# Kernel optimization log

Measured on AMD Instinct MI355X. Metric: run time of the kernel, lower is better.

Reference implementation:

```python
import math
import jax, jax.numpy as jnp
import numpy as np

N, S, D = 1024, 256, 256
C, R, CLASSES = 256, 64, 1000


def setup_inputs() -> dict:
    key = jax.random.key(0)
    ks = jax.random.split(key, 10)
    inv_sqrt_d = 1.0 / math.sqrt(D)
    return {
        "q": jax.random.normal(ks[0], (N, D), dtype=jnp.float32),
        "K": jax.random.normal(ks[1], (N, S, D), dtype=jnp.float32),
        "V": jax.random.normal(ks[2], (N, S, D), dtype=jnp.float32),
        "codebook": jax.random.normal(ks[3], (C, D), dtype=jnp.float32) * inv_sqrt_d,
        "residual_codebook": jax.random.normal(ks[4], (R, D), dtype=jnp.float32) * inv_sqrt_d,
        "Wq": jax.random.normal(ks[5], (D, D), dtype=jnp.float32) * inv_sqrt_d,
        "residual_logit": jnp.zeros((), dtype=jnp.float32),
        "Wc": jax.random.normal(ks[6], (CLASSES, D), dtype=jnp.float32) * inv_sqrt_d,
        "bc": jnp.zeros((CLASSES,), dtype=jnp.float32),
        "Wr": jax.random.normal(ks[7], (D, D), dtype=jnp.float32) * inv_sqrt_d,
        "br": jnp.zeros((D,), dtype=jnp.float32),
    }


def reference(q, K, V, codebook, residual_codebook, Wq, residual_logit, Wc, bc, Wr, br):
    scale = math.sqrt(q.shape[-1])
    q_proj = q @ Wq.T  # [N,D]

    # --- base codebook pass ---
    code_weights = jax.nn.softmax(jnp.einsum('nd,cd->nc', q_proj, codebook) / scale, axis=-1)
    slot_code_weights = jax.nn.softmax(jnp.einsum('nsd,cd->nsc', K, codebook) / scale, axis=-1)
    slot_code_summaries = jnp.einsum('nsc,nsd->ncd', slot_code_weights, V)
    base_summary = jnp.einsum('nc,ncd->nd', code_weights, slot_code_summaries)
    base_weights = jnp.einsum('nc,nsc->ns', code_weights, slot_code_weights)

    # --- residual quantization pass ---
    query_residual = q_proj - code_weights @ codebook
    slot_residual = K - jnp.einsum('nsc,cd->nsd', slot_code_weights, codebook)
    residual_code_weights = jax.nn.softmax(
        jnp.einsum('nd,rd->nr', query_residual, residual_codebook) / scale, axis=-1)
    residual_slot_code_weights = jax.nn.softmax(
        jnp.einsum('nsd,rd->nsr', slot_residual, residual_codebook) / scale, axis=-1)
    residual_slot_summaries = jnp.einsum('nsr,nsd->nrd', residual_slot_code_weights, V)
    residual_summary = jnp.einsum('nr,nrd->nd', residual_code_weights, residual_slot_summaries)
    residual_weights = jnp.einsum('nr,nsr->ns', residual_code_weights, residual_slot_code_weights)

    gate = jax.nn.sigmoid(residual_logit)
    summary = base_summary + gate * residual_summary
    effective_weights = (base_weights + gate * residual_weights) / (1.0 + gate)

    logits = summary @ Wc.T + bc
    recon = summary @ Wr.T + br
    return (logits, recon, effective_weights)
```

## Files before the change

kernel.cpp:

```cpp
#include <hip/hip_runtime.h>
#include <hip/hip_bf16.h>
#include <math.h>

#define N_   1024
#define S_   256
#define D_   256
#define C_   256
#define R_   64
#define CLS_ 1000
#define INV16 0.0625f

typedef unsigned short ushortT;
typedef unsigned int uint32;
typedef short bf8 __attribute__((ext_vector_type(8)));
typedef float f4 __attribute__((ext_vector_type(4)));

static __device__ __forceinline__ float bf2f(uint32 u){
  return __uint_as_float(u << 16);
}
static __device__ __forceinline__ ushortT f2bf(float f){
  uint32 x = __float_as_uint(f);
  uint32 r = x + 0x7FFFu + ((x >> 16) & 1u);
  return (ushortT)(r >> 16);
}
static __device__ __forceinline__ uint32 packbf(float a, float b){
  return ((uint32)f2bf(b) << 16) | (uint32)f2bf(a);
}
static __device__ __forceinline__ float wred_max(float v){
  for (int o = 32; o; o >>= 1) v = fmaxf(v, __shfl_xor(v, o));
  return v;
}
static __device__ __forceinline__ float wred_sum(float v){
  for (int o = 32; o; o >>= 1) v += __shfl_xor(v, o);
  return v;
}
static __device__ __forceinline__ int swz(int row, int colbyte){
  return row*512 + ((colbyte & ~15) ^ ((row & 7) << 4)) + (colbyte & 15);
}
static __device__ __forceinline__ int pkidx(int row, int col, int nfrag){
  int ks = col >> 5, hi = (col >> 3) & 3, e = col & 7;
  int frag = row >> 4, l15p = row & 15;
  return ((ks*nfrag + frag)*64 + hi*16 + l15p)*8 + e;
}

__global__ __launch_bounds__(256) void k0(const float* __restrict__ cb,
    const float* __restrict__ rcb, const float* __restrict__ Wc,
    const float* __restrict__ Wr, ushortT* __restrict__ a1pk,
    ushortT* __restrict__ Wcr_bf, float* __restrict__ MT_f32,
    ushortT* __restrict__ mtpk)
{
  __shared__ float rl[D_];
  int bid = blockIdx.x, t = threadIdx.x;
  int gtid = bid*256 + t;
  int stride = gridDim.x*256;
  for (int e = gtid; e < (C_ + R_)*D_; e += stride){
    int row = e >> 8, col = e & 255;
    float v = (row < C_) ? cb[e] : rcb[e - C_*D_];
    a1pk[pkidx(row, col, 20)] = f2bf(v);
  }
  for (int e = gtid; e < CLS_*D_; e += stride) Wcr_bf[e] = f2bf(Wc[e]);
  for (int e = gtid; e < D_*D_; e += stride)  Wcr_bf[CLS_*D_ + e] = f2bf(Wr[e]);
  for (int e = gtid; e < 24*D_; e += stride)  Wcr_bf[1256*D_ + e] = 0;

  if (bid < R_){
    rl[t] = rcb[bid*D_ + t];
    __syncthreads();
    float acc = 0.f;
    const float* crow = cb + t*D_;
    #pragma unroll 8
    for (int k = 0; k < D_; k += 4){
      float4 w = *(const float4*)(crow + k);
      acc += w.x*rl[k] + w.y*rl[k+1] + w.z*rl[k+2] + w.w*rl[k+3];
    }
    MT_f32[bid*C_ + t] = acc;
    mtpk[pkidx(bid, t, 4)] = f2bf(acc);
  }
}

#define G4 4
__global__ __launch_bounds__(256) void k1(const float* __restrict__ q,
    const float* __restrict__ cb, const float* __restrict__ rcb,
    const float* __restrict__ Wq, const float* __restrict__ MT_f32,
    float* __restrict__ cw_ws, float* __restrict__ rcw_ws)
{
  __shared__ float qv[G4][D_], qp[G4][D_], cwl[G4][C_];
  __shared__ float redA[G4][4], redB2[G4][4];
  int n0 = blockIdx.x*G4, t = threadIdx.x;
  #pragma unroll
  for (int g = 0; g < G4; g++) qv[g][t] = q[(n0+g)*D_ + t];
  __syncthreads();
  {
    float acc[G4] = {0.f,0.f,0.f,0.f};
    const float* wrow = Wq + t*D_;
    #pragma unroll 4
    for (int k = 0; k < D_; k += 4){
      float4 w = *(const float4*)(wrow + k);
      #pragma unroll
      for (int g = 0; g < G4; g++)
        acc[g] += qv[g][k]*w.x + qv[g][k+1]*w.y + qv[g][k+2]*w.z + qv[g][k+3]*w.w;
    }
    #pragma unroll
    for (int g = 0; g < G4; g++) qp[g][t] = acc[g];
  }
  __syncthreads();
  float L[G4] = {0.f,0.f,0.f,0.f};
  {
    const float* crow = cb + t*D_;
    #pragma unroll 4
    for (int k = 0; k < D_; k += 4){
      float4 w = *(const float4*)(crow + k);
      #pragma unroll
      for (int g = 0; g < G4; g++)
        L[g] += qp[g][k]*w.x + qp[g][k+1]*w.y + qp[g][k+2]*w.z + qp[g][k+3]*w.w;
    }
  }
  float m[G4], e[G4], s[G4];
  #pragma unroll
  for (int g = 0; g < G4; g++){ L[g] *= INV16; m[g] = wred_max(L[g]); }
  if ((t & 63) == 0)
    #pragma unroll
    for (int g = 0; g < G4; g++) redA[g][t >> 6] = m[g];
  __syncthreads();
  #pragma unroll
  for (int g = 0; g < G4; g++){
    m[g] = fmaxf(fmaxf(redA[g][0], redA[g][1]), fmaxf(redA[g][2], redA[g][3]));
    e[g] = __expf(L[g] - m[g]);
    s[g] = wred_sum(e[g]);
  }
  if ((t & 63) == 0)
    #pragma unroll
    for (int g = 0; g < G4; g++) redB2[g][t >> 6] = s[g];
  __syncthreads();
  #pragma unroll
  for (int g = 0; g < G4; g++){
    float ss = redB2[g][0] + redB2[g][1] + redB2[g][2] + redB2[g][3];
    float w = e[g] / ss;
    cwl[g][t] = w;
    cw_ws[(n0+g)*C_ + t] = w;
  }
  __syncthreads();
  if (t < R_){
    float qd[G4] = {0.f,0.f,0.f,0.f}, md[G4] = {0.f,0.f,0.f,0.f};
    const float* rrow = rcb + t*D_;
    const float* mrow = MT_f32 + t*C_;
    #pragma unroll 4
    for (int k = 0; k < D_; k += 4){
      float4 wv = *(const float4*)(rrow + k);
      float4 mv = *(const float4*)(mrow + k);
      #pragma unroll
      for (int g = 0; g < G4; g++){
        qd[g] += qp[g][k]*wv.x + qp[g][k+1]*wv.y + qp[g][k+2]*wv.z + qp[g][k+3]*wv.w;
        md[g] += cwl[g][k]*mv.x + cwl[g][k+1]*mv.y + cwl[g][k+2]*mv.z + cwl[g][k+3]*mv.w;
      }
    }
    #pragma unroll
    for (int g = 0; g < G4; g++){
      float Lr = (qd[g] - md[g]) * INV16;
      float mr = wred_max(Lr);
      float er = __expf(Lr - mr);
      float sr = wred_sum(er);
      rcw_ws[(n0+g)*R_ + t] = er / sr;
    }
  }
}

__global__ __launch_bounds__(256) void k2a(const float* __restrict__ Kt,
    const ushortT* __restrict__ a1pk, const ushortT* __restrict__ mtpk,
    const float* __restrict__ cw_ws, const float* __restrict__ rcw_ws,
    const float* __restrict__ rlogit, float* __restrict__ comb_ws,
    float* __restrict__ out_ew)
{
  __shared__ __align__(16) ushortT KW[64*256];
  __shared__ float redS[4][64], redW[4][64];

  int bx  = blockIdx.x;
  int n   = bx >> 2;
  int s0  = (bx & 3) * 64;
  int tid = threadIdx.x;
  int lane = tid & 63, w = tid >> 6;
  int l15 = lane & 15, l4 = lane >> 4;
  float gate  = 1.f / (1.f + __expf(-rlogit[0]));
  float inv1g = 1.f / (1.f + gate);

  const float* Kn = Kt + (size_t)n*S_*D_ + (size_t)s0*D_;

  #pragma unroll
  for (int j = 0; j < 8; j++){
    int ch = tid + j*256;
    int row = ch >> 5, blk = ch & 31;
    const float* src = Kn + row*D_ + blk*8;
    float4 a = *(const float4*)src;
    float4 b = *(const float4*)(src + 4);
    uint4 wv = {packbf(a.x,a.y), packbf(a.z,a.w), packbf(b.x,b.y), packbf(b.z,b.w)};
    *(uint4*)((char*)KW + swz(row, blk*16)) = wv;
  }
  __syncthreads();

  const ushortT* a1b = a1pk + (size_t)lane*8;
  bf8 bnxC[4], bnxR[4];
  #pragma unroll
  for (int f = 0; f < 4; f++){
    bnxC[f] = *(const bf8*)(a1b + (size_t)((w + 4*f)*64)*8);
    bnxR[f] = *(const bf8*)(a1b + (size_t)((16 + f)*64)*8);
  }
  f4 accC[4][4]; f4 accR[4];
  #pragma unroll
  for (int f = 0; f < 4; f++){
    accR[f] = (f4)0.f;
    #pragma unroll
    for (int sj = 0; sj < 4; sj++) accC[f][sj] = (f4)0.f;
  }
  #pragma unroll
  for (int ks = 0; ks < 8; ks++){
    bf8 kf0 = *(const bf8*)((const char*)KW + swz(     l15, ks*64 + l4*16));
    bf8 kf1 = *(const bf8*)((const char*)KW + swz(16 + l15, ks*64 + l4*16));
    bf8 kf2 = *(const bf8*)((const char*)KW + swz(32 + l15, ks*64 + l4*16));
    bf8 kf3 = *(const bf8*)((const char*)KW + swz(48 + l15, ks*64 + l4*16));
    bf8 kfw = *(const bf8*)((const char*)KW + swz(w*16 + l15, ks*64 + l4*16));
    #pragma unroll
    for (int f = 0; f < 4; f++){
      bf8 aC = bnxC[f], aR = bnxR[f];
      if (ks < 7){
        bnxC[f] = *(const bf8*)(a1b + (size_t)(((ks+1)*20 + w + 4*f)*64)*8);
        bnxR[f] = *(const bf8*)(a1b + (size_t)(((ks+1)*20 + 16 + f)*64)*8);
      }
      accC[f][0] = __builtin_amdgcn_mfma_f32_16x16x32_bf16(aC, kf0, accC[f][0], 0, 0, 0);
      accC[f][1] = __builtin_amdgcn_mfma_f32_16x16x32_bf16(aC, kf1, accC[f][1], 0, 0, 0);
      accC[f][2] = __builtin_amdgcn_mfma_f32_16x16x32_bf16(aC, kf2, accC[f][2], 0, 0, 0);
      accC[f][3] = __builtin_amdgcn_mfma_f32_16x16x32_bf16(aC, kf3, accC[f][3], 0, 0, 0);
      accR[f]    = __builtin_amdgcn_mfma_f32_16x16x32_bf16(aR, kfw, accR[f],    0, 0, 0);
    }
  }

  float4 cwv[4];
  #pragma unroll
  for (int f = 0; f < 4; f++)
    cwv[f] = *(const float4*)(cw_ws + n*C_ + (w + 4*f)*16 + l4*4);
  float se[4] = {0,0,0,0}, sb[4] = {0,0,0,0};
  #pragma unroll
  for (int f = 0; f < 4; f++)
    #pragma unroll
    for (int sj = 0; sj < 4; sj++){
      float e0 = __expf(accC[f][sj][0] * INV16);
      float e1 = __expf(accC[f][sj][1] * INV16);
      float e2 = __expf(accC[f][sj][2] * INV16);
      float e3 = __expf(accC[f][sj][3] * INV16);
      accC[f][sj][0] = e0; accC[f][sj][1] = e1;
      accC[f][sj][2] = e2; accC[f][sj][3] = e3;
      se[sj] += (e0 + e1) + (e2 + e3);
      sb[sj] += e0*cwv[f].x + e1*cwv[f].y + e2*cwv[f].z + e3*cwv[f].w;
    }
  #pragma unroll
  for (int sj = 0; sj < 4; sj++){
    se[sj] += __shfl_xor(se[sj], 16); se[sj] += __shfl_xor(se[sj], 32);
    sb[sj] += __shfl_xor(sb[sj], 16); sb[sj] += __shfl_xor(sb[sj], 32);
  }
  if (l4 == 0){
    #pragma unroll
    for (int sj = 0; sj < 4; sj++){
      redS[w][sj*16 + l15] = se[sj];
      redW[w][sj*16 + l15] = sb[sj];
    }
  }
  __syncthreads();

  float bw_q, rcp_q;
  {
    int sq = w*16 + l15;
    float sS = redS[0][sq] + redS[1][sq] + redS[2][sq] + redS[3][sq];
    float sW = redW[0][sq] + redW[1][sq] + redW[2][sq] + redW[3][sq];
    bw_q  = sW / sS;
    rcp_q = 1.f / sS;
  }
  #pragma unroll
  for (int f = 0; f < 4; f++){
    int cbyte = ((w + 4*f)*16 + l4*4) * 2;
    #pragma unroll
    for (int sj = 0; sj < 4; sj++){
      int s_ = sj*16 + l15;
      *(uint32*)((char*)KW + swz(s_, cbyte))     = packbf(accC[f][sj][0], accC[f][sj][1]);
      *(uint32*)((char*)KW + swz(s_, cbyte + 4)) = packbf(accC[f][sj][2], accC[f][sj][3]);
    }
  }
  __syncthreads();

  const ushortT* mtb = mtpk + (size_t)lane*8;
  bf8 mnx[4];
  #pragma unroll
  for (int fr = 0; fr < 4; fr++)
    mnx[fr] = *(const bf8*)(mtb + (size_t)(fr*64)*8);
  f4 wm[4];
  #pragma unroll
  for (int fr = 0; fr < 4; fr++) wm[fr] = (f4)0.f;
  #pragma unroll
  for (int ks = 0; ks < 8; ks++){
    bf8 wb = *(const bf8*)((const char*)KW + swz(w*16 + l15, ks*64 + l4*16));
    #pragma unroll
    for (int fr = 0; fr < 4; fr++){
      bf8 a = mnx[fr];
      if (ks < 7) mnx[fr] = *(const bf8*)(mtb + (size_t)(((ks+1)*4 + fr)*64)*8);
      wm[fr] = __builtin_amdgcn_mfma_f32_16x16x32_bf16(a, wb, wm[fr], 0, 0, 0);
    }
  }

  float4 rcwv[4];
  #pragma unroll
  for (int fr = 0; fr < 4; fr++)
    rcwv[fr] = *(const float4*)(rcw_ws + n*R_ + fr*16 + l4*4);
  float se3 = 0.f, sc3 = 0.f;
  #pragma unroll
  for (int fr = 0; fr < 4; fr++){
    float e0 = __expf((accR[fr][0] - wm[fr][0]*rcp_q) * INV16);
    float e1 = __expf((accR[fr][1] - wm[fr][1]*rcp_q) * INV16);
    float e2 = __expf((accR[fr][2] - wm[fr][2]*rcp_q) * INV16);
    float e3 = __expf((accR[fr][3] - wm[fr][3]*rcp_q) * INV16);
    se3 += (e0 + e1) + (e2 + e3);
    sc3 += e0*rcwv[fr].x + e1*rcwv[fr].y + e2*rcwv[fr].z + e3*rcwv[fr].w;
  }
  se3 += __shfl_xor(se3, 16); se3 += __shfl_xor(se3, 32);
  sc3 += __shfl_xor(sc3, 16); sc3 += __shfl_xor(sc3, 32);
  float comb = bw_q + gate * (sc3 / se3);
  if (l4 == 0){
    int sabs = n*S_ + s0 + w*16 + l15;
    out_ew[sabs]  = comb * inv1g;
    comb_ws[sabs] = comb;
  }
}

__global__ __launch_bounds__(256) void k2b(const float* __restrict__ Vt,
    const float* __restrict__ comb_ws, float* __restrict__ sum_ws)
{
  __shared__ float cl[S_];
  __shared__ float4 part[4][64];
  int n = blockIdx.x, tid = threadIdx.x;
  int lane = tid & 63, w = tid >> 6;
  cl[tid] = comb_ws[n*S_ + tid];
  __syncthreads();
  const float* Vn = Vt + (size_t)n*S_*D_ + (size_t)(w*64)*D_ + lane*4;
  float4 a0 = {0,0,0,0}, a1 = {0,0,0,0};
  #pragma unroll 8
  for (int j = 0; j < 64; j += 2){
    float4 v0 = *(const float4*)(Vn + (size_t)j*D_);
    float4 v1 = *(const float4*)(Vn + (size_t)(j+1)*D_);
    float c0 = cl[w*64 + j], c1 = cl[w*64 + j + 1];
    a0.x = fmaf(c0, v0.x, a0.x); a0.y = fmaf(c0, v0.y, a0.y);
    a0.z = fmaf(c0, v0.z, a0.z); a0.w = fmaf(c0, v0.w, a0.w);
    a1.x = fmaf(c1, v1.x, a1.x); a1.y = fmaf(c1, v1.y, a1.y);
    a1.z = fmaf(c1, v1.z, a1.z); a1.w = fmaf(c1, v1.w, a1.w);
  }
  float4 acc = {a0.x+a1.x, a0.y+a1.y, a0.z+a1.z, a0.w+a1.w};
  part[w][lane] = acc;
  __syncthreads();
  if (tid < 64){
    float4 p0 = part[0][tid], p1 = part[1][tid], p2 = part[2][tid], p3 = part[3][tid];
    float4 r = {p0.x+p1.x+p2.x+p3.x, p0.y+p1.y+p2.y+p3.y,
                p0.z+p1.z+p2.z+p3.z, p0.w+p1.w+p2.w+p3.w};
    *(float4*)(sum_ws + (size_t)n*D_ + tid*4) = r;
  }
}

__global__ __launch_bounds__(256) void k3(const float* __restrict__ sum_ws,
    const ushortT* __restrict__ Wcr_bf, const float* __restrict__ bc,
    const float* __restrict__ br, float* __restrict__ out)
{
  __shared__ __align__(16) ushortT Stile[64*256];
  int bx = blockIdx.x;
  int ot = bx >> 4;
  int nt = bx & 15;
  int tid = threadIdx.x;
  int lane = tid & 63, wid = tid >> 6;
  int l15 = lane & 15, l4 = lane >> 4;

  const float* Sp = sum_ws + (size_t)nt*64*D_;
  #pragma unroll
  for (int j = 0; j < 8; j++){
    int ch = tid + j*256;
    int row = ch >> 5, blk = ch & 31;
    const float* src = Sp + row*D_ + blk*8;
    float4 a = *(const float4*)src;
    float4 b = *(const float4*)(src + 4);
    uint4 wv = {packbf(a.x,a.y), packbf(a.z,a.w), packbf(b.x,b.y), packbf(b.z,b.w)};
    *(uint4*)((char*)Stile + swz(row, blk*16)) = wv;
  }
  __syncthreads();

  int o0 = ot*64 + wid*16;
  const ushortT* Ap = Wcr_bf + (size_t)(o0 + l15)*D_ + l4*8;
  f4 acc[4];
  #pragma unroll
  for (int j = 0; j < 4; j++) acc[j] = (f4)0.f;
  #pragma unroll
  for (int k = 0; k < 8; k++){
    bf8 a = *(const bf8*)(Ap + k*32);
    #pragma unroll
    for (int nj = 0; nj < 4; nj++){
      bf8 b = *(const bf8*)((const char*)Stile + swz(nj*16 + l15, k*64 + l4*16));
      acc[nj] = __builtin_amdgcn_mfma_f32_16x16x32_bf16(a, b, acc[nj], 0, 0, 0);
    }
  }
  int obase = o0 + l4*4;
  if (obase < 1256){
    float4 bias;
    if (obase < CLS_) bias = *(const float4*)(bc + obase);
    else              bias = *(const float4*)(br + (obase - CLS_));
    #pragma unroll
    for (int nj = 0; nj < 4; nj++){
      int nn = nt*64 + nj*16 + l15;
      float4 v = {acc[nj][0]+bias.x, acc[nj][1]+bias.y, acc[nj][2]+bias.z, acc[nj][3]+bias.w};
      if (obase < CLS_) *(float4*)(out + (size_t)nn*CLS_ + obase) = v;
      else              *(float4*)(out + (size_t)N_*CLS_ + (size_t)nn*D_ + (obase - CLS_)) = v;
    }
  }
}

extern "C" void kernel_launch(void* const* d_in, const int* in_sizes, int n_in,
                              void* d_out, int out_size, void* d_ws, size_t ws_size,
                              hipStream_t stream)
{
  const float* q    = (const float*)d_in[0];
  const float* Kt   = (const float*)d_in[1];
  const float* Vt   = (const float*)d_in[2];
  const float* cb   = (const float*)d_in[3];
  const float* rcb  = (const float*)d_in[4];
  const float* Wq   = (const float*)d_in[5];
  const float* rlg  = (const float*)d_in[6];
  const float* Wc   = (const float*)d_in[7];
  const float* bc   = (const float*)d_in[8];
  const float* Wr   = (const float*)d_in[9];
  const float* br   = (const float*)d_in[10];
  float* out = (float*)d_out;
  float* ws  = (float*)d_ws;

  float* cw_ws   = ws;
  float* rcw_ws  = ws + 262144;
  float* sum_ws  = ws + 327680;
  float* comb_ws = ws + 589824;
  float* MT_f32  = ws + 851968;
  ushortT* a1pk   = (ushortT*)(ws + 868352);
  ushortT* mtpk   = a1pk + (C_ + R_)*D_;
  ushortT* Wcr_bf = mtpk + R_*C_;

  float* out_logits = out;
  float* out_ew     = out + (size_t)N_*CLS_ + (size_t)N_*D_;

  k0 <<<128,   256, 0, stream>>>(cb, rcb, Wc, Wr, a1pk, Wcr_bf, MT_f32, mtpk);
  k1 <<<N_/G4, 256, 0, stream>>>(q, cb, rcb, Wq, MT_f32, cw_ws, rcw_ws);
  k2a<<<N_*4,  256, 0, stream>>>(Kt, a1pk, mtpk, cw_ws, rcw_ws, rlg, comb_ws, out_ew);
  k2b<<<N_,    256, 0, stream>>>(Vt, comb_ws, sum_ws);
  k3 <<<320,   256, 0, stream>>>(sum_ws, Wcr_bf, bc, br, out_logits);
}
```

Before: 234.4 us.

## Fuse V-weighted summary into k2a via atomics and repartition residual MFMA work

Removes the separate k2b kernel and the comb_ws round trip: each k2a block now multiplies its 64 slots' combined weights against V and atomically adds partial summaries into sum_ws, which k0 zero-initialises. The residual-code MFMAs are also repartitioned so each wave owns 16 residual codes across all 64 slots instead of 16 slots across all codes. A cross-wave reduction through shared memory with one extra barrier replaces the per-wave softmax normalisation. This saves a launch and a pass over comb_ws, at the cost of 4-way float atomics per output element and nondeterministic summation order.

After: 288.3 us. 23.0% more time.

```diff
diff --git a/kernel.cpp b/kernel.cpp
--- a/kernel.cpp
+++ b/kernel.cpp
@@ -47,7 +47,7 @@
     const float* __restrict__ rcb, const float* __restrict__ Wc,
     const float* __restrict__ Wr, ushortT* __restrict__ a1pk,
     ushortT* __restrict__ Wcr_bf, float* __restrict__ MT_f32,
-    ushortT* __restrict__ mtpk)
+    ushortT* __restrict__ mtpk, float* __restrict__ sum_ws)
 {
   __shared__ float rl[D_];
   int bid = blockIdx.x, t = threadIdx.x;
@@ -61,6 +61,7 @@
   for (int e = gtid; e < CLS_*D_; e += stride) Wcr_bf[e] = f2bf(Wc[e]);
   for (int e = gtid; e < D_*D_; e += stride)  Wcr_bf[CLS_*D_ + e] = f2bf(Wr[e]);
   for (int e = gtid; e < 24*D_; e += stride)  Wcr_bf[1256*D_ + e] = 0;
+  for (int e = gtid; e < N_*D_; e += stride)  sum_ws[e] = 0.f;
 
   if (bid < R_){
     rl[t] = rcb[bid*D_ + t];
@@ -165,10 +166,10 @@
 }
 
 __global__ __launch_bounds__(256) void k2a(const float* __restrict__ Kt,
-    const ushortT* __restrict__ a1pk, const ushortT* __restrict__ mtpk,
-    const float* __restrict__ cw_ws, const float* __restrict__ rcw_ws,
-    const float* __restrict__ rlogit, float* __restrict__ comb_ws,
-    float* __restrict__ out_ew)
+    const float* __restrict__ Vt, const ushortT* __restrict__ a1pk,
+    const ushortT* __restrict__ mtpk, const float* __restrict__ cw_ws,
+    const float* __restrict__ rcw_ws, const float* __restrict__ rlogit,
+    float* __restrict__ sum_ws, float* __restrict__ out_ew)
 {
   __shared__ __align__(16) ushortT KW[64*256];
   __shared__ float redS[4][64], redW[4][64];
@@ -184,6 +185,12 @@
 
   const float* Kn = Kt + (size_t)n*S_*D_ + (size_t)s0*D_;
 
+  const ushortT* aRb = a1pk + (size_t)((16 + w)*64 + lane)*8;
+  bf8 bR[8];
+  #pragma unroll
+  for (int ks = 0; ks < 8; ks++)
+    bR[ks] = *(const bf8*)(aRb + (size_t)(ks*20*64)*8);
+
   #pragma unroll
   for (int j = 0; j < 8; j++){
     int ch = tid + j*256;
@@ -197,12 +204,10 @@
   __syncthreads();
 
   const ushortT* a1b = a1pk + (size_t)lane*8;
-  bf8 bnxC[4], bnxR[4];
-  #pragma unroll
-  for (int f = 0; f < 4; f++){
+  bf8 bnxC[4];
+  #pragma unroll
+  for (int f = 0; f < 4; f++)
     bnxC[f] = *(const bf8*)(a1b + (size_t)((w + 4*f)*64)*8);
-    bnxR[f] = *(const bf8*)(a1b + (size_t)((16 + f)*64)*8);
-  }
   f4 accC[4][4]; f4 accR[4];
   #pragma unroll
   for (int f = 0; f < 4; f++){
@@ -216,21 +221,27 @@
     bf8 kf1 = *(const bf8*)((const char*)KW + swz(16 + l15, ks*64 + l4*16));
     bf8 kf2 = *(const bf8*)((const char*)KW + swz(32 + l15, ks*64 + l4*16));
     bf8 kf3 = *(const bf8*)((const char*)KW + swz(48 + l15, ks*64 + l4*16));
-    bf8 kfw = *(const bf8*)((const char*)KW + swz(w*16 + l15, ks*64 + l4*16));
     #pragma unroll
     for (int f = 0; f < 4; f++){
-      bf8 aC = bnxC[f], aR = bnxR[f];
-      if (ks < 7){
+      bf8 aC = bnxC[f];
+      if (ks < 7)
         bnxC[f] = *(const bf8*)(a1b + (size_t)(((ks+1)*20 + w + 4*f)*64)*8);
-        bnxR[f] = *(const bf8*)(a1b + (size_t)(((ks+1)*20 + 16 + f)*64)*8);
-      }
       accC[f][0] = __builtin_amdgcn_mfma_f32_16x16x32_bf16(aC, kf0, accC[f][0], 0, 0, 0);
       accC[f][1] = __builtin_amdgcn_mfma_f32_16x16x32_bf16(aC, kf1, accC[f][1], 0, 0, 0);
       accC[f][2] = __builtin_amdgcn_mfma_f32_16x16x32_bf16(aC, kf2, accC[f][2], 0, 0, 0);
       accC[f][3] = __builtin_amdgcn_mfma_f32_16x16x32_bf16(aC, kf3, accC[f][3], 0, 0, 0);
-      accR[f]    = __builtin_amdgcn_mfma_f32_16x16x32_bf16(aR, kfw, accR[f],    0, 0, 0);
-    }
-  }
+    }
+    accR[0] = __builtin_amdgcn_mfma_f32_16x16x32_bf16(bR[ks], kf0, accR[0], 0, 0, 0);
+    accR[1] = __builtin_amdgcn_mfma_f32_16x16x32_bf16(bR[ks], kf1, accR[1], 0, 0, 0);
+    accR[2] = __builtin_amdgcn_mfma_f32_16x16x32_bf16(bR[ks], kf2, accR[2], 0, 0, 0);
+    accR[3] = __builtin_amdgcn_mfma_f32_16x16x32_bf16(bR[ks], kf3, accR[3], 0, 0, 0);
+  }
+
+  const ushortT* mtb = mtpk + (size_t)(w*64 + lane)*8;
+  bf8 mnx[8];
+  #pragma unroll
+  for (int ks = 0; ks < 8; ks++)
+    mnx[ks] = *(const bf8*)(mtb + (size_t)(ks*4*64)*8);
 
   float4 cwv[4];
   #pragma unroll
@@ -264,13 +275,18 @@
   }
   __syncthreads();
 
-  float bw_q, rcp_q;
+  float rcp[4];
+  #pragma unroll
+  for (int sj = 0; sj < 4; sj++){
+    int s_ = sj*16 + l15;
+    rcp[sj] = 1.f / (redS[0][s_] + redS[1][s_] + redS[2][s_] + redS[3][s_]);
+  }
+  float bw_q;
   {
     int sq = w*16 + l15;
     float sS = redS[0][sq] + redS[1][sq] + redS[2][sq] + redS[3][sq];
     float sW = redW[0][sq] + redW[1][sq] + redW[2][sq] + redW[3][sq];
-    bw_q  = sW / sS;
-    rcp_q = 1.f / sS;
+    bw_q = sW / sS;
   }
   #pragma unroll
   for (int f = 0; f < 4; f++){
@@ -284,78 +300,68 @@
   }
   __syncthreads();
 
-  const ushortT* mtb = mtpk + (size_t)lane*8;
-  bf8 mnx[4];
-  #pragma unroll
-  for (int fr = 0; fr < 4; fr++)
-    mnx[fr] = *(const bf8*)(mtb + (size_t)(fr*64)*8);
   f4 wm[4];
   #pragma unroll
-  for (int fr = 0; fr < 4; fr++) wm[fr] = (f4)0.f;
+  for (int sj = 0; sj < 4; sj++) wm[sj] = (f4)0.f;
   #pragma unroll
   for (int ks = 0; ks < 8; ks++){
-    bf8 wb = *(const bf8*)((const char*)KW + swz(w*16 + l15, ks*64 + l4*16));
-    #pragma unroll
-    for (int fr = 0; fr < 4; fr++){
-      bf8 a = mnx[fr];
-      if (ks < 7) mnx[fr] = *(const bf8*)(mtb + (size_t)(((ks+1)*4 + fr)*64)*8);
-      wm[fr] = __builtin_amdgcn_mfma_f32_16x16x32_bf16(a, wb, wm[fr], 0, 0, 0);
-    }
-  }
-
-  float4 rcwv[4];
-  #pragma unroll
-  for (int fr = 0; fr < 4; fr++)
-    rcwv[fr] = *(const float4*)(rcw_ws + n*R_ + fr*16 + l4*4);
-  float se3 = 0.f, sc3 = 0.f;
-  #pragma unroll
-  for (int fr = 0; fr < 4; fr++){
-    float e0 = __expf((accR[fr][0] - wm[fr][0]*rcp_q) * INV16);
-    float e1 = __expf((accR[fr][1] - wm[fr][1]*rcp_q) * INV16);
-    float e2 = __expf((accR[fr][2] - wm[fr][2]*rcp_q) * INV16);
-    float e3 = __expf((accR[fr][3] - wm[fr][3]*rcp_q) * INV16);
-    se3 += (e0 + e1) + (e2 + e3);
-    sc3 += e0*rcwv[fr].x + e1*rcwv[fr].y + e2*rcwv[fr].z + e3*rcwv[fr].w;
-  }
-  se3 += __shfl_xor(se3, 16); se3 += __shfl_xor(se3, 32);
-  sc3 += __shfl_xor(sc3, 16); sc3 += __shfl_xor(sc3, 32);
-  float comb = bw_q + gate * (sc3 / se3);
+    bf8 wb0 = *(const bf8*)((const char*)KW + swz(     l15, ks*64 + l4*16));
+    bf8 wb1 = *(const bf8*)((const char*)KW + swz(16 + l15, ks*64 + l4*16));
+    bf8 wb2 = *(const bf8*)((const char*)KW + swz(32 + l15, ks*64 + l4*16));
+    bf8 wb3 = *(const bf8*)((const char*)KW + swz(48 + l15, ks*64 + l4*16));
+    wm[0] = __builtin_amdgcn_mfma_f32_16x16x32_bf16(mnx[ks], wb0, wm[0], 0, 0, 0);
+    wm[1] = __builtin_amdgcn_mfma_f32_16x16x32_bf16(mnx[ks], wb1, wm[1], 0, 0, 0);
+    wm[2] = __builtin_amdgcn_mfma_f32_16x16x32_bf16(mnx[ks], wb2, wm[2], 0, 0, 0);
+    wm[3] = __builtin_amdgcn_mfma_f32_16x16x32_bf16(mnx[ks], wb3, wm[3], 0, 0, 0);
+  }
+
+  float4 rcwv = *(const float4*)(rcw_ws + n*R_ + w*16 + l4*4);
+  float se3[4], sc3[4];
+  #pragma unroll
+  for (int sj = 0; sj < 4; sj++){
+    float e0 = __expf((accR[sj][0] - wm[sj][0]*rcp[sj]) * INV16);
+    float e1 = __expf((accR[sj][1] - wm[sj][1]*rcp[sj]) * INV16);
+    float e2 = __expf((accR[sj][2] - wm[sj][2]*rcp[sj]) * INV16);
+    float e3 = __expf((accR[sj][3] - wm[sj][3]*rcp[sj]) * INV16);
+    float s_e = (e0 + e1) + (e2 + e3);
+    float s_c = e0*rcwv.x + e1*rcwv.y + e2*rcwv.z + e3*rcwv.w;
+    s_e += __shfl_xor(s_e, 16); s_e += __shfl_xor(s_e, 32);
+    s_c += __shfl_xor(s_c, 16); s_c += __shfl_xor(s_c, 32);
+    se3[sj] = s_e; sc3[sj] = s_c;
+  }
   if (l4 == 0){
-    int sabs = n*S_ + s0 + w*16 + l15;
-    out_ew[sabs]  = comb * inv1g;
-    comb_ws[sabs] = comb;
-  }
-}
-
-__global__ __launch_bounds__(256) void k2b(const float* __restrict__ Vt,
-    const float* __restrict__ comb_ws, float* __restrict__ sum_ws)
-{
-  __shared__ float cl[S_];
-  __shared__ float4 part[4][64];
-  int n = blockIdx.x, tid = threadIdx.x;
-  int lane = tid & 63, w = tid >> 6;
-  cl[tid] = comb_ws[n*S_ + tid];
-  __syncthreads();
-  const float* Vn = Vt + (size_t)n*S_*D_ + (size_t)(w*64)*D_ + lane*4;
-  float4 a0 = {0,0,0,0}, a1 = {0,0,0,0};
-  #pragma unroll 8
-  for (int j = 0; j < 64; j += 2){
-    float4 v0 = *(const float4*)(Vn + (size_t)j*D_);
-    float4 v1 = *(const float4*)(Vn + (size_t)(j+1)*D_);
-    float c0 = cl[w*64 + j], c1 = cl[w*64 + j + 1];
-    a0.x = fmaf(c0, v0.x, a0.x); a0.y = fmaf(c0, v0.y, a0.y);
-    a0.z = fmaf(c0, v0.z, a0.z); a0.w = fmaf(c0, v0.w, a0.w);
-    a1.x = fmaf(c1, v1.x, a1.x); a1.y = fmaf(c1, v1.y, a1.y);
-    a1.z = fmaf(c1, v1.z, a1.z); a1.w = fmaf(c1, v1.w, a1.w);
-  }
-  float4 acc = {a0.x+a1.x, a0.y+a1.y, a0.z+a1.z, a0.w+a1.w};
-  part[w][lane] = acc;
-  __syncthreads();
-  if (tid < 64){
-    float4 p0 = part[0][tid], p1 = part[1][tid], p2 = part[2][tid], p3 = part[3][tid];
-    float4 r = {p0.x+p1.x+p2.x+p3.x, p0.y+p1.y+p2.y+p3.y,
-                p0.z+p1.z+p2.z+p3.z, p0.w+p1.w+p2.w+p3.w};
-    *(float4*)(sum_ws + (size_t)n*D_ + tid*4) = r;
+    #pragma unroll
+    for (int sj = 0; sj < 4; sj++){
+      redS[w][sj*16 + l15] = se3[sj];
+      redW[w][sj*16 + l15] = sc3[sj];
+    }
+  }
+  __syncthreads();
+
+  float comb;
+  {
+    int sq = w*16 + l15;
+    float sS = redS[0][sq] + redS[1][sq] + redS[2][sq] + redS[3][sq];
+    float sW = redW[0][sq] + redW[1][sq] + redW[2][sq] + redW[3][sq];
+    comb = bw_q + gate * (sW / sS);
+    if (l4 == 0) out_ew[n*S_ + s0 + sq] = comb * inv1g;
+  }
+
+  {
+    const float* vp = Vt + (size_t)n*S_*D_ + (size_t)(s0 + w*16)*D_ + lane*4;
+    float4 sacc = {0.f, 0.f, 0.f, 0.f};
+    #pragma unroll
+    for (int j = 0; j < 16; j++){
+      float cj = __shfl(comb, j);
+      float4 v = *(const float4*)(vp + (size_t)j*D_);
+      sacc.x = fmaf(cj, v.x, sacc.x); sacc.y = fmaf(cj, v.y, sacc.y);
+      sacc.z = fmaf(cj, v.z, sacc.z); sacc.w = fmaf(cj, v.w, sacc.w);
+    }
+    float* dst = sum_ws + (size_t)n*D_ + lane*4;
+    atomicAdd(dst + 0, sacc.x);
+    atomicAdd(dst + 1, sacc.y);
+    atomicAdd(dst + 2, sacc.z);
+    atomicAdd(dst + 3, sacc.w);
   }
 }
 
@@ -434,18 +440,16 @@
   float* cw_ws   = ws;
   float* rcw_ws  = ws + 262144;
   float* sum_ws  = ws + 327680;
-  float* comb_ws = ws + 589824;
-  float* MT_f32  = ws + 851968;
-  ushortT* a1pk   = (ushortT*)(ws + 868352);
+  float* MT_f32  = ws + 589824;
+  ushortT* a1pk   = (ushortT*)(ws + 606208);
   ushortT* mtpk   = a1pk + (C_ + R_)*D_;
   ushortT* Wcr_bf = mtpk + R_*C_;
 
   float* out_logits = out;
   float* out_ew     = out + (size_t)N_*CLS_ + (size_t)N_*D_;
 
-  k0 <<<128,   256, 0, stream>>>(cb, rcb, Wc, Wr, a1pk, Wcr_bf, MT_f32, mtpk);
+  k0 <<<128,   256, 0, stream>>>(cb, rcb, Wc, Wr, a1pk, Wcr_bf, MT_f32, mtpk, sum_ws);
   k1 <<<N_/G4, 256, 0, stream>>>(q, cb, rcb, Wq, MT_f32, cw_ws, rcw_ws);
-  k2a<<<N_*4,  256, 0, stream>>>(Kt, a1pk, mtpk, cw_ws, rcw_ws, rlg, comb_ws, out_ew);
-  k2b<<<N_,    256, 0, stream>>>(Vt, comb_ws, sum_ws);
+  k2a<<<N_*4,  256, 0, stream>>>(Kt, Vt, a1pk, mtpk, cw_ws, rcw_ws, rlg, sum_ws, out_ew);
   k3 <<<320,   256, 0, stream>>>(sum_ws, Wcr_bf, bc, br, out_logits);
 }
```

## Loop k2a over slot tiles with double-buffered LDS K prefetch

Applied to the files above, without the earlier changes.

k2a now launches one block per query row instead of four, looping over the four 64-slot tiles. The next tile of K is loaded from global memory into registers during the current tile's MFMA loop, then converted to bf16 and stored into a second LDS buffer. The per-row cw/rcw vectors are loaded once per block instead of once per tile. This hides global-load latency behind compute, but the doubled LDS footprint and a quarter of the blocks may reduce occupancy and latency hiding across blocks.

Result: slower. 493.4 us (+110.4%).

```diff
diff --git a/kernel.cpp b/kernel.cpp
--- a/kernel.cpp
+++ b/kernel.cpp
@@ -170,160 +170,207 @@
     const float* __restrict__ rlogit, float* __restrict__ comb_ws,
     float* __restrict__ out_ew)
 {
-  __shared__ __align__(16) ushortT KW[64*256];
+  __shared__ __align__(16) ushortT KW[2][64*256];
   __shared__ float redS[4][64], redW[4][64];
 
-  int bx  = blockIdx.x;
-  int n   = bx >> 2;
-  int s0  = (bx & 3) * 64;
+  int n   = blockIdx.x;
   int tid = threadIdx.x;
   int lane = tid & 63, w = tid >> 6;
   int l15 = lane & 15, l4 = lane >> 4;
   float gate  = 1.f / (1.f + __expf(-rlogit[0]));
   float inv1g = 1.f / (1.f + gate);
 
-  const float* Kn = Kt + (size_t)n*S_*D_ + (size_t)s0*D_;
+  const float* KnBase = Kt + (size_t)n*S_*D_;
+
+  float4 cwv[4];
+  #pragma unroll
+  for (int f = 0; f < 4; f++)
+    cwv[f] = *(const float4*)(cw_ws + n*C_ + (w + 4*f)*16 + l4*4);
+  float4 rcwv[4];
+  #pragma unroll
+  for (int fr = 0; fr < 4; fr++)
+    rcwv[fr] = *(const float4*)(rcw_ws + n*R_ + fr*16 + l4*4);
 
   #pragma unroll
   for (int j = 0; j < 8; j++){
     int ch = tid + j*256;
     int row = ch >> 5, blk = ch & 31;
-    const float* src = Kn + row*D_ + blk*8;
+    const float* src = KnBase + row*D_ + blk*8;
     float4 a = *(const float4*)src;
     float4 b = *(const float4*)(src + 4);
     uint4 wv = {packbf(a.x,a.y), packbf(a.z,a.w), packbf(b.x,b.y), packbf(b.z,b.w)};
-    *(uint4*)((char*)KW + swz(row, blk*16)) = wv;
-  }
-  __syncthreads();
-
-  const ushortT* a1b = a1pk + (size_t)lane*8;
-  bf8 bnxC[4], bnxR[4];
-  #pragma unroll
-  for (int f = 0; f < 4; f++){
-    bnxC[f] = *(const bf8*)(a1b + (size_t)((w + 4*f)*64)*8);
-    bnxR[f] = *(const bf8*)(a1b + (size_t)((16 + f)*64)*8);
-  }
-  f4 accC[4][4]; f4 accR[4];
-  #pragma unroll
-  for (int f = 0; f < 4; f++){
-    accR[f] = (f4)0.f;
-    #pragma unroll
-    for (int sj = 0; sj < 4; sj++) accC[f][sj] = (f4)0.f;
-  }
-  #pragma unroll
-  for (int ks = 0; ks < 8; ks++){
-    bf8 kf0 = *(const bf8*)((const char*)KW + swz(     l15, ks*64 + l4*16));
-    bf8 kf1 = *(const bf8*)((const char*)KW + swz(16 + l15, ks*64 + l4*16));
-    bf8 kf2 = *(const bf8*)((const char*)KW + swz(32 + l15, ks*64 + l4*16));
-    bf8 kf3 = *(const bf8*)((const char*)KW + swz(48 + l15, ks*64 + l4*16));
-    bf8 kfw = *(const bf8*)((const char*)KW + swz(w*16 + l15, ks*64 + l4*16));
+    *(uint4*)((char*)KW[0] + swz(row, blk*16)) = wv;
+  }
+  __syncthreads();
+
+  #pragma unroll 1
+  for (int t = 0; t < 4; t++){
+    int s0 = t*64;
+    const char* KWc = (const char*)KW[t & 1];
+    char*       KWn = (char*)KW[(t & 1) ^ 1];
+    const float* Knx = KnBase + (size_t)(s0 + 64)*D_;
+    bool stage = (t < 3);
+
+    const ushortT* a1b = a1pk + (size_t)lane*8;
+    bf8 bnxC[4], bnxR[4];
     #pragma unroll
     for (int f = 0; f < 4; f++){
-      bf8 aC = bnxC[f], aR = bnxR[f];
-      if (ks < 7){
-        bnxC[f] = *(const bf8*)(a1b + (size_t)(((ks+1)*20 + w + 4*f)*64)*8);
-        bnxR[f] = *(const bf8*)(a1b + (size_t)(((ks+1)*20 + 16 + f)*64)*8);
-      }
-      accC[f][0] = __builtin_amdgcn_mfma_f32_16x16x32_bf16(aC, kf0, accC[f][0], 0, 0, 0);
-      accC[f][1] = __builtin_amdgcn_mfma_f32_16x16x32_bf16(aC, kf1, accC[f][1], 0, 0, 0);
-      accC[f][2] = __builtin_amdgcn_mfma_f32_16x16x32_bf16(aC, kf2, accC[f][2], 0, 0, 0);
-      accC[f][3] = __builtin_amdgcn_mfma_f32_16x16x32_bf16(aC, kf3, accC[f][3], 0, 0, 0);
-      accR[f]    = __builtin_amdgcn_mfma_f32_16x16x32_bf16(aR, kfw, accR[f],    0, 0, 0);
-    }
-  }
-
-  float4 cwv[4];
-  #pragma unroll
-  for (int f = 0; f < 4; f++)
-    cwv[f] = *(const float4*)(cw_ws + n*C_ + (w + 4*f)*16 + l4*4);
-  float se[4] = {0,0,0,0}, sb[4] = {0,0,0,0};
-  #pragma unroll
-  for (int f = 0; f < 4; f++)
+      bnxC[f] = *(const bf8*)(a1b + (size_t)((w + 4*f)*64)*8);
+      bnxR[f] = *(const bf8*)(a1b + (size_t)((16 + f)*64)*8);
+    }
+    f4 accC[4][4]; f4 accR[4];
+    #pragma unroll
+    for (int f = 0; f < 4; f++){
+      accR[f] = (f4)0.f;
+      #pragma unroll
+      for (int sj = 0; sj < 4; sj++) accC[f][sj] = (f4)0.f;
+    }
+    float4 stg[2][2];
+    #pragma unroll
+    for (int ks = 0; ks < 8; ks++){
+      if (stage){
+        if (ks >= 2){
+          int j = ks - 2;
+          int ch = tid + j*256;
+          int row = ch >> 5, blk = ch & 31;
+          uint4 wv = {packbf(stg[j & 1][0].x, stg[j & 1][0].y),
+                      packbf(stg[j & 1][0].z, stg[j & 1][0].w),
+                      packbf(stg[j & 1][1].x, stg[j & 1][1].y),
+                      packbf(stg[j & 1][1].z, stg[j & 1][1].w)};
+          *(uint4*)(KWn + swz(row, blk*16)) = wv;
+        }
+        {
+          int ch = tid + ks*256;
+          int row = ch >> 5, blk = ch & 31;
+          const float* src = Knx + row*D_ + blk*8;
+          stg[ks & 1][0] = *(const float4*)src;
+          stg[ks & 1][1] = *(const float4*)(src + 4);
+        }
+      }
+      bf8 kf0 = *(const bf8*)(KWc + swz(     l15, ks*64 + l4*16));
+      bf8 kf1 = *(const bf8*)(KWc + swz(16 + l15, ks*64 + l4*16));
+      bf8 kf2 = *(const bf8*)(KWc + swz(32 + l15, ks*64 + l4*16));
+      bf8 kf3 = *(const bf8*)(KWc + swz(48 + l15, ks*64 + l4*16));
+      bf8 kfw = *(const bf8*)(KWc + swz(w*16 + l15, ks*64 + l4*16));
+      #pragma unroll
+      for (int f = 0; f < 4; f++){
+        bf8 aC = bnxC[f], aR = bnxR[f];
+        if (ks < 7){
+          bnxC[f] = *(const bf8*)(a1b + (size_t)(((ks+1)*20 + w + 4*f)*64)*8);
+          bnxR[f] = *(const bf8*)(a1b + (size_t)(((ks+1)*20 + 16 + f)*64)*8);
+        }
+        accC[f][0] = __builtin_amdgcn_mfma_f32_16x16x32_bf16(aC, kf0, accC[f][0], 0, 0, 0);
+        accC[f][1] = __builtin_amdgcn_mfma_f32_16x16x32_bf16(aC, kf1, accC[f][1], 0, 0, 0);
+        accC[f][2] = __builtin_amdgcn_mfma_f32_16x16x32_bf16(aC, kf2, accC[f][2], 0, 0, 0);
+        accC[f][3] = __builtin_amdgcn_mfma_f32_16x16x32_bf16(aC, kf3, accC[f][3], 0, 0, 0);
+        accR[f]    = __builtin_amdgcn_mfma_f32_16x16x32_bf16(aR, kfw, accR[f],    0, 0, 0);
+      }
+    }
+    if (stage){
+      #pragma unroll
+      for (int j = 6; j < 8; j++){
+        int ch = tid + j*256;
+        int row = ch >> 5, blk = ch & 31;
+        uint4 wv = {packbf(stg[j & 1][0].x, stg[j & 1][0].y),
+                    packbf(stg[j & 1][0].z, stg[j & 1][0].w),
+                    packbf(stg[j & 1][1].x, stg[j & 1][1].y),
+                    packbf(stg[j & 1][1].z, stg[j & 1][1].w)};
+        *(uint4*)(KWn + swz(row, blk*16)) = wv;
+      }
+    }
+
+    float se[4] = {0,0,0,0}, sb[4] = {0,0,0,0};
+    #pragma unroll
+    for (int f = 0; f < 4; f++)
+      #pragma unroll
+      for (int sj = 0; sj < 4; sj++){
+        float e0 = __expf(accC[f][sj][0] * INV16);
+        float e1 = __expf(accC[f][sj][1] * INV16);
+        float e2 = __expf(accC[f][sj][2] * INV16);
+        float e3 = __expf(accC[f][sj][3] * INV16);
+        accC[f][sj][0] = e0; accC[f][sj][1] = e1;
+        accC[f][sj][2] = e2; accC[f][sj][3] = e3;
+        se[sj] += (e0 + e1) + (e2 + e3);
+        sb[sj] += e0*cwv[f].x + e1*cwv[f].y + e2*cwv[f].z + e3*cwv[f].w;
+      }
     #pragma unroll
     for (int sj = 0; sj < 4; sj++){
-      float e0 = __expf(accC[f][sj][0] * INV16);
-      float e1 = __expf(accC[f][sj][1] * INV16);
-      float e2 = __expf(accC[f][sj][2] * INV16);
-      float e3 = __expf(accC[f][sj][3] * INV16);
-      accC[f][sj][0] = e0; accC[f][sj][1] = e1;
-      accC[f][sj][2] = e2; accC[f][sj][3] = e3;
-      se[sj] += (e0 + e1) + (e2 + e3);
-      sb[sj] += e0*cwv[f].x + e1*cwv[f].y + e2*cwv[f].z + e3*cwv[f].w;
-    }
-  #pragma unroll
-  for (int sj = 0; sj < 4; sj++){
-    se[sj] += __shfl_xor(se[sj], 16); se[sj] += __shfl_xor(se[sj], 32);
-    sb[sj] += __shfl_xor(sb[sj], 16); sb[sj] += __shfl_xor(sb[sj], 32);
-  }
-  if (l4 == 0){
-    #pragma unroll
-    for (int sj = 0; sj < 4; sj++){
-      redS[w][sj*16 + l15] = se[sj];
-      redW[w][sj*16 + l15] = sb[sj];
-    }
-  }
-  __syncthreads();
-
-  float bw_q, rcp_q;
-  {
-    int sq = w*16 + l15;
-    float sS = redS[0][sq] + redS[1][sq] + redS[2][sq] + redS[3][sq];
-    float sW = redW[0][sq] + redW[1][sq] + redW[2][sq] + redW[3][sq];
-    bw_q  = sW / sS;
-    rcp_q = 1.f / sS;
-  }
-  #pragma unroll
-  for (int f = 0; f < 4; f++){
-    int cbyte = ((w + 4*f)*16 + l4*4) * 2;
+      se[sj] += __shfl_xor(se[sj], 16); se[sj] += __shfl_xor(se[sj], 32);
+      sb[sj] += __shfl_xor(sb[sj], 16); sb[sj] += __shfl_xor(sb[sj], 32);
+    }
+    if (l4 == 0){
+      #pragma unroll
+      for (int sj = 0; sj < 4; sj++){
+        redS[w][sj*16 + l15] = se[sj];
+        redW[w][sj*16 + l15] = sb[sj];
+      }
+    }
+    __syncthreads();
+
+    float rcp[4];
     #pragma unroll
     for (int sj = 0; sj < 4; sj++){
       int s_ = sj*16 + l15;
-      *(uint32*)((char*)KW + swz(s_, cbyte))     = packbf(accC[f][sj][0], accC[f][sj][1]);
-      *(uint32*)((char*)KW + swz(s_, cbyte + 4)) = packbf(accC[f][sj][2], accC[f][sj][3]);
-    }
-  }
-  __syncthreads();
-
-  const ushortT* mtb = mtpk + (size_t)lane*8;
-  bf8 mnx[4];
-  #pragma unroll
-  for (int fr = 0; fr < 4; fr++)
-    mnx[fr] = *(const bf8*)(mtb + (size_t)(fr*64)*8);
-  f4 wm[4];
-  #pragma unroll
-  for (int fr = 0; fr < 4; fr++) wm[fr] = (f4)0.f;
-  #pragma unroll
-  for (int ks = 0; ks < 8; ks++){
-    bf8 wb = *(const bf8*)((const char*)KW + swz(w*16 + l15, ks*64 + l4*16));
+      rcp[sj] = 1.f / (redS[0][s_] + redS[1][s_] + redS[2][s_] + redS[3][s_]);
+    }
+    float bw_q, rcp_q;
+    {
+      int sq = w*16 + l15;
+      float sS = redS[0][sq] + redS[1][sq] + redS[2][sq] + redS[3][sq];
+      float sW = redW[0][sq] + redW[1][sq] + redW[2][sq] + redW[3][sq];
+      bw_q  = sW / sS;
+      rcp_q = 1.f / sS;
+    }
+    #pragma unroll
+    for (int f = 0; f < 4; f++){
+      int cbyte = ((w + 4*f)*16 + l4*4) * 2;
+      #pragma unroll
+      for (int sj = 0; sj < 4; sj++){
+        int s_ = sj*16 + l15;
+        *(uint32*)((char*)KWc + swz(s_, cbyte))     = packbf(accC[f][sj][0], accC[f][sj][1]);
+        *(uint32*)((char*)KWc + swz(s_, cbyte + 4)) = packbf(accC[f][sj][2], accC[f][sj][3]);
+      }
+    }
+    __syncthreads();
+
+    const ushortT* mtb = mtpk + (size_t)lane*8;
+    bf8 mnx[4];
+    #pragma unroll
+    for (int fr = 0; fr < 4; fr++)
+      mnx[fr] = *(const bf8*)(mtb + (size_t)(fr*64)*8);
+    f4 wm[4];
+    #pragma unroll
+    for (int fr = 0; fr < 4; fr++) wm[fr] = (f4)0.f;
+    #pragma unroll
+    for (int ks = 0; ks < 8; ks++){
+      bf8 wb = *(const bf8*)(KWc + swz(w*16 + l15, ks*64 + l4*16));
+      #pragma unroll
+      for (int fr = 0; fr < 4; fr++){
+        bf8 a = mnx[fr];
+        if (ks < 7) mnx[fr] = *(const bf8*)(mtb + (size_t)(((ks+1)*4 + fr)*64)*8);
+        wm[fr] = __builtin_amdgcn_mfma_f32_16x16x32_bf16(a, wb, wm[fr], 0, 0, 0);
+      }
+    }
+
+    float se3 = 0.f, sc3 = 0.f;
     #pragma unroll
     for (int fr = 0; fr < 4; fr++){
-      bf8 a = mnx[fr];
-      if (ks < 7) mnx[fr] = *(const bf8*)(mtb + (size_t)(((ks+1)*4 + fr)*64)*8);
-      wm[fr] = __builtin_amdgcn_mfma_f32_16x16x32_bf16(a, wb, wm[fr], 0, 0, 0);
-    }
-  }
-
-  float4 rcwv[4];
-  #pragma unroll
-  for (int fr = 0; fr < 4; fr++)
-    rcwv[fr] = *(const float4*)(rcw_ws + n*R_ + fr*16 + l4*4);
-  float se3 = 0.f, sc3 = 0.f;
-  #pragma unroll
-  for (int fr = 0; fr < 4; fr++){
-    float e0 = __expf((accR[fr][0] - wm[fr][0]*rcp_q) * INV16);
-    float e1 = __expf((accR[fr][1] - wm[fr][1]*rcp_q) * INV16);
-    float e2 = __expf((accR[fr][2] - wm[fr][2]*rcp_q) * INV16);
-    float e3 = __expf((accR[fr][3] - wm[fr][3]*rcp_q) * INV16);
-    se3 += (e0 + e1) + (e2 + e3);
-    sc3 += e0*rcwv[fr].x + e1*rcwv[fr].y + e2*rcwv[fr].z + e3*rcwv[fr].w;
-  }
-  se3 += __shfl_xor(se3, 16); se3 += __shfl_xor(se3, 32);
-  sc3 += __shfl_xor(sc3, 16); sc3 += __shfl_xor(sc3, 32);
-  float comb = bw_q + gate * (sc3 / se3);
-  if (l4 == 0){
-    int sabs = n*S_ + s0 + w*16 + l15;
-    out_ew[sabs]  = comb * inv1g;
-    comb_ws[sabs] = comb;
+      float e0 = __expf((accR[fr][0] - wm[fr][0]*rcp_q) * INV16);
+      float e1 = __expf((accR[fr][1] - wm[fr][1]*rcp_q) * INV16);
+      float e2 = __expf((accR[fr][2] - wm[fr][2]*rcp_q) * INV16);
+      float e3 = __expf((accR[fr][3] - wm[fr][3]*rcp_q) * INV16);
+      se3 += (e0 + e1) + (e2 + e3);
+      sc3 += e0*rcwv[fr].x + e1*rcwv[fr].y + e2*rcwv[fr].z + e3*rcwv[fr].w;
+    }
+    se3 += __shfl_xor(se3, 16); se3 += __shfl_xor(se3, 32);
+    sc3 += __shfl_xor(sc3, 16); sc3 += __shfl_xor(sc3, 32);
+    float comb = bw_q + gate * (sc3 / se3);
+    if (l4 == 0){
+      int sabs = n*S_ + s0 + w*16 + l15;
+      out_ew[sabs]  = comb * inv1g;
+      comb_ws[sabs] = comb;
+    }
+    if (t < 3) __syncthreads();
   }
 }
 
@@ -445,7 +492,7 @@
 
   k0 <<<128,   256, 0, stream>>>(cb, rcb, Wc, Wr, a1pk, Wcr_bf, MT_f32, mtpk);
   k1 <<<N_/G4, 256, 0, stream>>>(q, cb, rcb, Wq, MT_f32, cw_ws, rcw_ws);
-  k2a<<<N_*4,  256, 0, stream>>>(Kt, a1pk, mtpk, cw_ws, rcw_ws, rlg, comb_ws, out_ew);
+  k2a<<<N_,    256, 0, stream>>>(Kt, a1pk, mtpk, cw_ws, rcw_ws, rlg, comb_ws, out_ew);
   k2b<<<N_,    256, 0, stream>>>(Vt, comb_ws, sum_ws);
   k3 <<<320,   256, 0, stream>>>(sum_ws, Wcr_bf, bc, br, out_logits);
 }
```
